# Kernel tuning notes

Measured on AMD Instinct MI355X. Metric: run time of the kernel, lower is better.

Reference implementation:

```python
import jax, jax.numpy as jnp
import numpy as np

B, TQ, TKV, D, H = 4, 1024, 1024, 1024, 16
HD = D // H  # head_size = 64
EPS = 1e-5


def setup_inputs() -> dict:
    key = jax.random.key(0)
    ks = jax.random.split(key, 5)
    s = 0.02
    return {
        "x_q": jax.random.normal(ks[0], (B, TQ, D), jnp.float32),
        "x_kv": jax.random.normal(ks[1], (B, TKV, D), jnp.float32),
        "Wq": jax.random.normal(ks[2], (D, 2 * D), jnp.float32) * s,
        "Wkv": jax.random.normal(ks[3], (D, 3 * D), jnp.float32) * s,
        "Wc": jax.random.normal(ks[4], (D, D), jnp.float32) * s,
        "qn1": jnp.ones((HD,), jnp.float32),
        "kn1": jnp.ones((HD,), jnp.float32),
        "qn2": jnp.ones((HD,), jnp.float32),
        "kn2": jnp.ones((HD,), jnp.float32),
        "gn_w": jnp.ones((D,), jnp.float32),
        "gn_b": jnp.zeros((D,), jnp.float32),
        "lmb": jnp.full((1, H, 1, 1), -4.0, jnp.float32),
    }


def _rms(x, w):
    # RMSNorm over last dim (head_size), eps=1e-5, learned scale w
    return x * jax.lax.rsqrt(jnp.mean(x * x, axis=-1, keepdims=True) + EPS) * w


def _heads(t, T):
    # (B,T,D) -> (B,H,T,HD)
    return t.reshape(B, T, H, HD).transpose(0, 2, 1, 3)


def _attn(q, k, v):
    att = jnp.einsum('bhqd,bhkd->bhqk', q, k) * (1.0 / np.sqrt(HD))
    att = jax.nn.softmax(att, axis=-1)
    return jnp.einsum('bhqk,bhkd->bhqd', att, v)


def reference(x_q, x_kv, Wq, Wkv, Wc, qn1, kn1, qn2, kn2, gn_w, gn_b, lmb):
    q1, q2 = jnp.split(x_q @ Wq, 2, axis=-1)
    k1, k2, v = jnp.split(x_kv @ Wkv, 3, axis=-1)
    q1 = _rms(_heads(q1, TQ), qn1)
    q2 = _rms(_heads(q2, TQ), qn2)
    k1 = _rms(_heads(k1, TKV), kn1)
    k2 = _rms(_heads(k2, TKV), kn2)
    v = _heads(v, TKV)
    y = _attn(q1, k1, v) - jax.nn.softplus(lmb) * _attn(q2, k2, v)  # (B,H,TQ,HD)
    # GroupNorm(n_head groups over n_embd channels), input (B,C,TQ):
    # per (batch, head) stats over (TQ, HD)
    mu = jnp.mean(y, axis=(2, 3), keepdims=True)
    var = jnp.var(y, axis=(2, 3), keepdims=True)
    yn = (y - mu) * jax.lax.rsqrt(var + EPS)
    yn = yn * gn_w.reshape(1, H, 1, HD) + gn_b.reshape(1, H, 1, HD)
    y = yn.transpose(0, 2, 1, 3).reshape(B, TQ, D)
    return y @ Wc
```

## Files before the change

### kernel.cpp

```cpp
#include <hip/hip_runtime.h>
#include <cstdint>
#include <cstddef>

#define B_ 4
#define TQ_ 1024
#define TKV_ 1024
#define D_ 1024
#define H_ 16
#define HD_ 64

typedef __bf16 bf16_t;
typedef bf16_t bf16x4 __attribute__((ext_vector_type(4)));
typedef bf16_t bf16x8 __attribute__((ext_vector_type(8)));
typedef float f32x4 __attribute__((ext_vector_type(4)));

#if __has_builtin(__builtin_amdgcn_exp2f)
#define EXP2F __builtin_amdgcn_exp2f
#else
#define EXP2F exp2f
#endif

__device__ __forceinline__ bf16_t to_bf16(float f) {
  uint32_t u = __builtin_bit_cast(uint32_t, f);
  u += 0x7fffu + ((u >> 16) & 1u);
  uint16_t h = (uint16_t)(u >> 16);
  return __builtin_bit_cast(bf16_t, h);
}
__device__ __forceinline__ float bf2f(bf16_t b) {
  uint32_t u = ((uint32_t)__builtin_bit_cast(uint16_t, b)) << 16;
  return __builtin_bit_cast(float, u);
}
__device__ __forceinline__ uint32_t pack_bf16_trunc(float lo, float hi) {
  return __builtin_amdgcn_perm(__builtin_bit_cast(uint32_t, hi),
                               __builtin_bit_cast(uint32_t, lo), 0x07060302u);
}
__device__ __forceinline__ void gload_lds16(const void* g, void* l) {
  __builtin_amdgcn_global_load_lds((const __attribute__((address_space(1))) void*)g,
                                   (__attribute__((address_space(3))) void*)l, 16, 0, 0);
}

__global__ __launch_bounds__(256) void k_prep(const float* __restrict__ xq,
                                              const float* __restrict__ xkv,
                                              const float* __restrict__ Wq,
                                              const float* __restrict__ Wkv,
                                              const float* __restrict__ Wc,
                                              bf16_t* __restrict__ oq,
                                              bf16_t* __restrict__ okv,
                                              bf16_t* __restrict__ Wqt,
                                              bf16_t* __restrict__ Wkvt,
                                              bf16_t* __restrict__ Wct,
                                              float* __restrict__ part) {
  int blk = blockIdx.x;
  if (blk == 0 && threadIdx.x < 128) part[threadIdx.x] = 0.f;
  if (blk < 8192) {
    const float* in = (blk < 4096) ? xq : xkv;
    bf16_t* out = (blk < 4096) ? oq : okv;
    int i = (blk & 4095) * 256 + threadIdx.x;
    float4 v = ((const float4*)in)[i];
    bf16x4 o = {to_bf16(v.x), to_bf16(v.y), to_bf16(v.z), to_bf16(v.w)};
    *(bf16x4*)(out + (size_t)i * 4) = o;
  } else {
    __shared__ float tile[32][33];
    int t = blk - 8192;
    int x = t % 192, yb = t / 192;
    const float* in;
    bf16_t* out;
    int C, c0;
    if (x < 64) { in = Wq; out = Wqt; C = 2048; c0 = x * 32; }
    else if (x < 160) { in = Wkv; out = Wkvt; C = 3072; c0 = (x - 64) * 32; }
    else { in = Wc; out = Wct; C = 1024; c0 = (x - 160) * 32; }
    int r0 = yb * 32;
    int tx = threadIdx.x & 31, ty = threadIdx.x >> 5;
#pragma unroll
    for (int i = 0; i < 4; i++)
      tile[ty + i * 8][tx] = in[(size_t)(r0 + ty + i * 8) * C + c0 + tx];
    __syncthreads();
#pragma unroll
    for (int i = 0; i < 4; i++) {
      int rr = ty + i * 8;
      out[(size_t)(c0 + rr) * 1024 + r0 + tx] = to_bf16(tile[tx][rr]);
    }
  }
}

__global__ __launch_bounds__(256, 2) void k_gemm_qkv(const bf16_t* __restrict__ xq,
                                                     const bf16_t* __restrict__ xkv,
                                                     const bf16_t* __restrict__ Wqt,
                                                     const bf16_t* __restrict__ Wkvt,
                                                     const float* __restrict__ kn1,
                                                     const float* __restrict__ kn2,
                                                     bf16_t* __restrict__ q12,
                                                     bf16_t* __restrict__ k1h,
                                                     bf16_t* __restrict__ k2h,
                                                     bf16_t* __restrict__ vt) {
  __shared__ bf16_t As[128 * 32];
  __shared__ bf16_t Bs[128 * 32];
  const int tid = threadIdx.x;
  const int wave = tid >> 6, lane = tid & 63;
  const int ln = lane & 15, lq = lane >> 4;

  const int fid = blockIdx.x;
  const int xcd = fid & 7, l = fid >> 3;
  bool isq;
  int xb, yb;
  if (l < 64) {
    isq = true;
    xb = (xcd & 3) * 4 + (l & 3);
    yb = (xcd >> 2) * 16 + (l >> 2);
  } else {
    isq = false;
    int l2 = l - 64;
    xb = (xcd & 3) * 6 + l2 % 6;
    yb = (xcd >> 2) * 16 + l2 / 6;
  }
  const bf16_t* A = isq ? xq : xkv;
  const bf16_t* Bt = isq ? Wqt : Wkvt;
  const int n0 = xb * 128, m0 = yb * 128;
  const int wm = (wave >> 1) * 64, wn = (wave & 1) * 64;
  f32x4 acc[4][4];
#pragma unroll
  for (int i = 0; i < 4; i++)
#pragma unroll
    for (int j = 0; j < 4; j++) acc[i][j] = (f32x4){0.f, 0.f, 0.f, 0.f};

  for (int k0 = 0; k0 < 1024; k0 += 32) {
#pragma unroll
    for (int rnd = 0; rnd < 2; rnd++) {
      int c = rnd * 256 + tid;
      int row = c >> 2, col = (c & 3) * 8;
      int ldsoff = (rnd * 256 + wave * 64) * 16;
      gload_lds16(A + (size_t)(m0 + row) * 1024 + k0 + col, (char*)As + ldsoff);
      gload_lds16(Bt + (size_t)(n0 + row) * 1024 + k0 + col, (char*)Bs + ldsoff);
    }
    asm volatile("s_waitcnt vmcnt(0)" ::: "memory");
    __syncthreads();
    bf16x8 af[4], bfr[4];
#pragma unroll
    for (int i = 0; i < 4; i++) {
      af[i] = *(const bf16x8*)(As + (wm + i * 16 + ln) * 32 + lq * 8);
      bfr[i] = *(const bf16x8*)(Bs + (wn + i * 16 + ln) * 32 + lq * 8);
    }
#pragma unroll
    for (int i = 0; i < 4; i++)
#pragma unroll
      for (int j = 0; j < 4; j++)
        acc[i][j] = __builtin_amdgcn_mfma_f32_16x16x32_bf16(af[i], bfr[j], acc[i][j], 0, 0, 0);
    __syncthreads();
  }

  if (isq) {
#pragma unroll
    for (int i = 0; i < 4; i++)
#pragma unroll
      for (int j = 0; j < 4; j++)
#pragma unroll
        for (int r = 0; r < 4; r++) {
          int row = m0 + wm + i * 16 + lq * 4 + r;
          int col = n0 + wn + j * 16 + ln;
          q12[(size_t)row * 2048 + col] = to_bf16(acc[i][j][r]);
        }
  } else {
    const int col0 = n0 + wn;
    const int part3 = col0 >> 10;
    const int h = (col0 >> 6) & 15;
    const int b = m0 >> 10;
    const int bh = b * 16 + h;
    if (part3 < 2) {
      const float* kn = part3 ? kn2 : kn1;
      bf16_t* dst = part3 ? k2h : k1h;
      float kw[4];
#pragma unroll
      for (int j = 0; j < 4; j++) kw[j] = kn[j * 16 + ln];
#pragma unroll
      for (int i = 0; i < 4; i++)
#pragma unroll
        for (int r = 0; r < 4; r++) {
          float ss = 0.f;
#pragma unroll
          for (int j = 0; j < 4; j++) ss += acc[i][j][r] * acc[i][j][r];
          ss += __shfl_xor(ss, 1, 64);
          ss += __shfl_xor(ss, 2, 64);
          ss += __shfl_xor(ss, 4, 64);
          ss += __shfl_xor(ss, 8, 64);
          float rstd = rsqrtf(ss * (1.f / 64.f) + 1e-5f);
          int m = m0 + wm + i * 16 + lq * 4 + r;
          int t = m & 1023;
          size_t base = ((size_t)bh * 1024 + t) * 64;
#pragma unroll
          for (int j = 0; j < 4; j++)
            dst[base + j * 16 + ln] = to_bf16(acc[i][j][r] * rstd * kw[j]);
        }
    } else {
      bf16_t* obase = vt + (size_t)bh * 65536;
#pragma unroll
      for (int i = 0; i < 4; i++) {
        int t0 = (m0 & 1023) + wm + i * 16 + lq * 4;
#pragma unroll
        for (int j = 0; j < 4; j++) {
          bf16x4 pv;
#pragma unroll
          for (int r = 0; r < 4; r++) pv[r] = to_bf16(acc[i][j][r]);
          *(bf16x4*)(obase + (size_t)(j * 16 + ln) * 1024 + t0) = pv;
        }
      }
    }
  }
}

__global__ __launch_bounds__(256, 2) void k_gemm64(const bf16_t* __restrict__ A,
                                                   const bf16_t* __restrict__ Bt,
                                                   float* __restrict__ C, int N, int K) {
  __shared__ bf16_t As[128 * 32];
  __shared__ bf16_t Bs[64 * 32];
  const int tid = threadIdx.x;
  const int wave = tid >> 6, lane = tid & 63;
  const int ln = lane & 15, lq = lane >> 4;
  const int fid = blockIdx.x;
  const int xcd = fid & 7, l = fid >> 3;
  const int lx = l & 1, ly = (l >> 1) & 15, yh = l >> 5;
  const int n0 = (xcd * 2 + lx) * 64;
  const int m0 = (yh * 16 + ly) * 128;
  const int wm = wave * 32;
  f32x4 acc[2][4];
#pragma unroll
  for (int i = 0; i < 2; i++)
#pragma unroll
    for (int j = 0; j < 4; j++) acc[i][j] = (f32x4){0.f, 0.f, 0.f, 0.f};

  for (int k0 = 0; k0 < K; k0 += 32) {
#pragma unroll
    for (int rnd = 0; rnd < 2; rnd++) {
      int c = rnd * 256 + tid;
      int row = c >> 2, col = (c & 3) * 8;
      int ldsoff = (rnd * 256 + wave * 64) * 16;
      gload_lds16(A + (size_t)(m0 + row) * K + k0 + col, (char*)As + ldsoff);
    }
    {
      int row = tid >> 2, col = (tid & 3) * 8;
      int ldsoff = (wave * 64) * 16;
      gload_lds16(Bt + (size_t)(n0 + row) * K + k0 + col, (char*)Bs + ldsoff);
    }
    asm volatile("s_waitcnt vmcnt(0)" ::: "memory");
    __syncthreads();
    bf16x8 af[2], bfr[4];
#pragma unroll
    for (int i = 0; i < 2; i++)
      af[i] = *(const bf16x8*)(As + (wm + i * 16 + ln) * 32 + lq * 8);
#pragma unroll
    for (int j = 0; j < 4; j++)
      bfr[j] = *(const bf16x8*)(Bs + (j * 16 + ln) * 32 + lq * 8);
#pragma unroll
    for (int i = 0; i < 2; i++)
#pragma unroll
      for (int j = 0; j < 4; j++)
        acc[i][j] = __builtin_amdgcn_mfma_f32_16x16x32_bf16(af[i], bfr[j], acc[i][j], 0, 0, 0);
    __syncthreads();
  }
#pragma unroll
  for (int i = 0; i < 2; i++)
#pragma unroll
    for (int j = 0; j < 4; j++)
#pragma unroll
      for (int r = 0; r < 4; r++) {
        int row = m0 + wm + i * 16 + lq * 4 + r;
        int col = n0 + j * 16 + ln;
        C[(size_t)row * N + col] = acc[i][j][r];
      }
}

__global__ __launch_bounds__(256, 4) void k_attn2(const bf16_t* __restrict__ q12,
                                                  const bf16_t* __restrict__ k1h,
                                                  const bf16_t* __restrict__ k2h,
                                                  const bf16_t* __restrict__ vt,
                                                  const float* __restrict__ qn1,
                                                  const float* __restrict__ qn2,
                                                  const float* __restrict__ lmb,
                                                  bf16_t* __restrict__ y,
                                                  float* __restrict__ part) {
  __shared__ bf16_t Ks[2][4096];
  __shared__ bf16_t Vs[4096];
  const int tid = threadIdx.x;
  const int wave = tid >> 6, lane = tid & 63;
  const int ln = lane & 15, lq = lane >> 4;
  const int swz = ln & 7;
  const int bh = blockIdx.x;
  const int b = bh >> 4, h = bh & 15;
  const int q0 = blockIdx.y * 64 + wave * 16;
  const bf16_t* kb[2] = {k1h + (size_t)bh * 65536, k2h + (size_t)bh * 65536};
  const bf16_t* vb = vt + (size_t)bh * 65536;

  bf16x8 qf[2][2];
#pragma unroll
  for (int st = 0; st < 2; st++)
#pragma unroll
    for (int ks = 0; ks < 2; ks++)
      qf[st][ks] = *(const bf16x8*)(q12 + (size_t)(b * 1024 + q0 + ln) * 2048 + st * 1024 +
                                    h * 64 + ks * 32 + lq * 8);
#pragma unroll
  for (int st = 0; st < 2; st++) {
    const float* qn = st ? qn2 : qn1;
    float ssq = 0.f;
#pragma unroll
    for (int ks = 0; ks < 2; ks++)
#pragma unroll
      for (int j = 0; j < 8; j++) {
        float v = bf2f(qf[st][ks][j]);
        ssq += v * v;
      }
    ssq += __shfl_xor(ssq, 16, 64);
    ssq += __shfl_xor(ssq, 32, 64);
    float rr = rsqrtf(ssq * (1.f / 64.f) + 1e-5f) * (0.125f * 1.44269504f);
#pragma unroll
    for (int ks = 0; ks < 2; ks++)
#pragma unroll
      for (int j = 0; j < 8; j++)
        qf[st][ks][j] = to_bf16(bf2f(qf[st][ks][j]) * rr * qn[ks * 32 + lq * 8 + j]);
  }

  f32x4 O[2][4];
  float lp[2] = {0.f, 0.f};
#pragma unroll
  for (int st = 0; st < 2; st++)
#pragma unroll
    for (int nt = 0; nt < 4; nt++) O[st][nt] = (f32x4){0.f, 0.f, 0.f, 0.f};

  for (int kv0 = 0; kv0 < TKV_; kv0 += 64) {
    __syncthreads();
#pragma unroll
    for (int r = 0; r < 6; r++) {
      int a = r >> 1, r2 = r & 1;
      int g = r2 * 256 + tid;
      int row = g >> 3;
      int blk = (g & 7) ^ (row & 7);
      const bf16_t* src = (a < 2) ? (kb[a] + (size_t)(kv0 + row) * 64 + blk * 8)
                                  : (vb + (size_t)row * 1024 + kv0 + blk * 8);
      char* dst = (a < 2) ? ((char*)Ks + a * 8192) : (char*)Vs;
      gload_lds16(src, dst + (r2 * 256 + wave * 64) * 16);
    }
    asm volatile("s_waitcnt vmcnt(0)" ::: "memory");
    __syncthreads();

#pragma unroll
    for (int st = 0; st < 2; st++) {
      bf16x8 kf[2][4];
#pragma unroll
      for (int ks = 0; ks < 2; ks++)
#pragma unroll
        for (int t = 0; t < 4; t++)
          kf[ks][t] = *(const bf16x8*)(&Ks[st][((t * 16 + ln) * 8 + ((4 * ks + lq) ^ swz)) * 8]);
      f32x4 s[4];
#pragma unroll
      for (int t = 0; t < 4; t++) s[t] = (f32x4){0.f, 0.f, 0.f, 0.f};
#pragma unroll
      for (int ks = 0; ks < 2; ks++)
#pragma unroll
        for (int t = 0; t < 4; t++)
          s[t] = __builtin_amdgcn_mfma_f32_16x16x32_bf16(kf[ks][t], qf[st][ks], s[t], 0, 0, 0);
      uint32_t pfu[2][4];
      float l = 0.f;
#pragma unroll
      for (int t = 0; t < 4; t++) {
        float e0 = EXP2F(s[t][0]), e1 = EXP2F(s[t][1]);
        float e2 = EXP2F(s[t][2]), e3 = EXP2F(s[t][3]);
        l += (e0 + e1) + (e2 + e3);
        pfu[t >> 1][(t & 1) * 2] = pack_bf16_trunc(e0, e1);
        pfu[t >> 1][(t & 1) * 2 + 1] = pack_bf16_trunc(e2, e3);
      }
      lp[st] += l;
#pragma unroll
      for (int u = 0; u < 2; u++) {
        bf16x8 pf = __builtin_bit_cast(bf16x8, *(uint4*)pfu[u]);
#pragma unroll
        for (int nt = 0; nt < 4; nt++) {
          uint2 lo = *(const uint2*)(Vs + ((nt * 16 + ln) * 8 + ((u * 4 + (lq >> 1)) ^ swz)) * 8 +
                                     (lq & 1) * 4);
          uint2 hi = *(const uint2*)(Vs + ((nt * 16 + ln) * 8 + ((u * 4 + 2 + (lq >> 1)) ^ swz)) * 8 +
                                     (lq & 1) * 4);
          uint4 vq = {lo.x, lo.y, hi.x, hi.y};
          bf16x8 vfrag = __builtin_bit_cast(bf16x8, vq);
          O[st][nt] = __builtin_amdgcn_mfma_f32_16x16x32_bf16(pf, vfrag, O[st][nt], 0, 0, 0);
        }
      }
    }
  }

  float c = log1pf(__expf(lmb[h]));
  float linv[2][4];
#pragma unroll
  for (int st = 0; st < 2; st++) {
    float l = lp[st];
    l += __shfl_xor(l, 16, 64);
    l += __shfl_xor(l, 32, 64);
#pragma unroll
    for (int r = 0; r < 4; r++) linv[st][r] = 1.f / __shfl(l, lq * 4 + r, 64);
  }
  float s_acc = 0.f, ss_acc = 0.f;
#pragma unroll
  for (int nt = 0; nt < 4; nt++)
#pragma unroll
    for (int r = 0; r < 4; r++) {
      size_t a = ((size_t)bh * TQ_ + q0 + lq * 4 + r) * 64 + nt * 16 + ln;
      float val = O[0][nt][r] * linv[0][r] - c * O[1][nt][r] * linv[1][r];
      s_acc += val;
      ss_acc += val * val;
      y[a] = to_bf16(val);
    }
#pragma unroll
  for (int m = 1; m < 64; m <<= 1) {
    s_acc += __shfl_xor(s_acc, m, 64);
    ss_acc += __shfl_xor(ss_acc, m, 64);
  }
  if (lane == 0) {
    atomicAdd(&part[bh * 2], s_acc);
    atomicAdd(&part[bh * 2 + 1], ss_acc);
  }
}

__global__ __launch_bounds__(256) void k_gn_apply(const bf16_t* __restrict__ y,
                                                  const float* __restrict__ part,
                                                  const float* __restrict__ gw,
                                                  const float* __restrict__ gb,
                                                  bf16_t* __restrict__ yn) {
  int idx = blockIdx.x * 256 + threadIdx.x;
  int i = idx * 8;
  int bh = i >> 16;
  int h = bh & 15, b = bh >> 4;
  float S = part[bh * 2], SS = part[bh * 2 + 1];
  float mean = S * (1.f / 65536.f);
  float var = SS * (1.f / 65536.f) - mean * mean;
  float rstd = rsqrtf(var + 1e-5f);
  bf16x8 a = *(const bf16x8*)(y + i);
  int rem = i & 65535;
  int t = rem >> 6, d = rem & 63;
  bf16x8 o;
#pragma unroll
  for (int j = 0; j < 8; j++) {
    float f = (bf2f(a[j]) - mean) * rstd * gw[h * 64 + d + j] + gb[h * 64 + d + j];
    o[j] = to_bf16(f);
  }
  *(bf16x8*)(yn + ((size_t)(b * 1024 + t)) * 1024 + h * 64 + d) = o;
}

extern "C" void kernel_launch(void* const* d_in, const int* in_sizes, int n_in,
                              void* d_out, int out_size, void* d_ws, size_t ws_size,
                              hipStream_t stream) {
  const float* x_q = (const float*)d_in[0];
  const float* x_kv = (const float*)d_in[1];
  const float* Wq = (const float*)d_in[2];
  const float* Wkv = (const float*)d_in[3];
  const float* Wc = (const float*)d_in[4];
  const float* qn1 = (const float*)d_in[5];
  const float* kn1 = (const float*)d_in[6];
  const float* qn2 = (const float*)d_in[7];
  const float* kn2 = (const float*)d_in[8];
  const float* gn_w = (const float*)d_in[9];
  const float* gn_b = (const float*)d_in[10];
  const float* lmb = (const float*)d_in[11];

  const size_t MB = (size_t)1 << 20;
  char* ws = (char*)d_ws;
  bf16_t* xq_bf = (bf16_t*)(ws + 0 * MB);
  bf16_t* xkv_bf = (bf16_t*)(ws + 8 * MB);
  bf16_t* Wqt = (bf16_t*)(ws + 16 * MB);
  bf16_t* Wkvt = (bf16_t*)(ws + 20 * MB);
  bf16_t* Wct = (bf16_t*)(ws + 26 * MB);
  bf16_t* q12 = (bf16_t*)(ws + 28 * MB);
  bf16_t* k1h = (bf16_t*)(ws + 44 * MB);
  bf16_t* k2h = (bf16_t*)(ws + 52 * MB);
  bf16_t* vt = (bf16_t*)(ws + 60 * MB);
  bf16_t* y = (bf16_t*)(ws + 68 * MB);
  bf16_t* yn = (bf16_t*)(ws + 76 * MB);
  float* part = (float*)(ws + 84 * MB);

  k_prep<<<14336, 256, 0, stream>>>(x_q, x_kv, Wq, Wkv, Wc, xq_bf, xkv_bf, Wqt, Wkvt, Wct,
                                    part);
  k_gemm_qkv<<<1280, 256, 0, stream>>>(xq_bf, xkv_bf, Wqt, Wkvt, kn1, kn2, q12, k1h, k2h,
                                       vt);
  k_attn2<<<dim3(64, 16), 256, 0, stream>>>(q12, k1h, k2h, vt, qn1, qn2, lmb, y, part);
  k_gn_apply<<<2048, 256, 0, stream>>>(y, part, gn_w, gn_b, yn);
  k_gemm64<<<512, 256, 0, stream>>>(yn, Wct, (float*)d_out, 1024, 1024);
}
```

Before: 268.6 us.

## Double per-wave query rows in attention and pre-permute V for single LDS reads

Each attention wave now handles 32 query rows instead of 16, so every K and V tile staged in shared memory is reused across two query sub-tiles, and the grid is halved to match. The V-transpose writer in the QKV GEMM stores columns in a permuted order so the attention kernel can fetch each V fragment with one 16-byte LDS read instead of two 8-byte reads, with V fragments hoisted out of the score loop. GroupNorm partial sums are first reduced across waves in shared memory, leaving one atomic per block. The trade-off is more registers per thread (occupancy hint lowered from 4 to 2) and fewer blocks available to fill the GPU.

Result: faster. 238.3 us (-11.3%).

```diff
diff --git a/kernel.cpp b/kernel.cpp
--- a/kernel.cpp
+++ b/kernel.cpp
@@ -195,12 +195,13 @@
 #pragma unroll
       for (int i = 0; i < 4; i++) {
         int t0 = (m0 & 1023) + wm + i * 16 + lq * 4;
+        int tp = (t0 & ~31) | (((t0 >> 2) & 3) << 3) | (((t0 >> 4) & 1) << 2);
 #pragma unroll
         for (int j = 0; j < 4; j++) {
           bf16x4 pv;
 #pragma unroll
           for (int r = 0; r < 4; r++) pv[r] = to_bf16(acc[i][j][r]);
-          *(bf16x4*)(obase + (size_t)(j * 16 + ln) * 1024 + t0) = pv;
+          *(bf16x4*)(obase + (size_t)(j * 16 + ln) * 1024 + tp) = pv;
         }
       }
     }
@@ -268,7 +269,7 @@
       }
 }
 
-__global__ __launch_bounds__(256, 4) void k_attn2(const bf16_t* __restrict__ q12,
+__global__ __launch_bounds__(256, 2) void k_attn2(const bf16_t* __restrict__ q12,
                                                   const bf16_t* __restrict__ k1h,
                                                   const bf16_t* __restrict__ k2h,
                                                   const bf16_t* __restrict__ vt,
@@ -279,50 +280,57 @@
                                                   float* __restrict__ part) {
   __shared__ bf16_t Ks[2][4096];
   __shared__ bf16_t Vs[4096];
+  __shared__ float red[8];
   const int tid = threadIdx.x;
   const int wave = tid >> 6, lane = tid & 63;
   const int ln = lane & 15, lq = lane >> 4;
   const int swz = ln & 7;
   const int bh = blockIdx.x;
   const int b = bh >> 4, h = bh & 15;
-  const int q0 = blockIdx.y * 64 + wave * 16;
+  const int q0 = blockIdx.y * 128 + wave * 32;
   const bf16_t* kb[2] = {k1h + (size_t)bh * 65536, k2h + (size_t)bh * 65536};
   const bf16_t* vb = vt + (size_t)bh * 65536;
 
-  bf16x8 qf[2][2];
+  bf16x8 qf[2][2][2];
 #pragma unroll
   for (int st = 0; st < 2; st++)
 #pragma unroll
-    for (int ks = 0; ks < 2; ks++)
-      qf[st][ks] = *(const bf16x8*)(q12 + (size_t)(b * 1024 + q0 + ln) * 2048 + st * 1024 +
-                                    h * 64 + ks * 32 + lq * 8);
-#pragma unroll
-  for (int st = 0; st < 2; st++) {
-    const float* qn = st ? qn2 : qn1;
-    float ssq = 0.f;
-#pragma unroll
-    for (int ks = 0; ks < 2; ks++)
-#pragma unroll
-      for (int j = 0; j < 8; j++) {
-        float v = bf2f(qf[st][ks][j]);
-        ssq += v * v;
-      }
-    ssq += __shfl_xor(ssq, 16, 64);
-    ssq += __shfl_xor(ssq, 32, 64);
-    float rr = rsqrtf(ssq * (1.f / 64.f) + 1e-5f) * (0.125f * 1.44269504f);
-#pragma unroll
-    for (int ks = 0; ks < 2; ks++)
-#pragma unroll
-      for (int j = 0; j < 8; j++)
-        qf[st][ks][j] = to_bf16(bf2f(qf[st][ks][j]) * rr * qn[ks * 32 + lq * 8 + j]);
-  }
-
-  f32x4 O[2][4];
-  float lp[2] = {0.f, 0.f};
+    for (int mt = 0; mt < 2; mt++)
+#pragma unroll
+      for (int ks = 0; ks < 2; ks++)
+        qf[st][mt][ks] = *(const bf16x8*)(q12 + (size_t)(b * 1024 + q0 + mt * 16 + ln) * 2048 +
+                                          st * 1024 + h * 64 + ks * 32 + lq * 8);
 #pragma unroll
   for (int st = 0; st < 2; st++)
 #pragma unroll
-    for (int nt = 0; nt < 4; nt++) O[st][nt] = (f32x4){0.f, 0.f, 0.f, 0.f};
+    for (int mt = 0; mt < 2; mt++) {
+      const float* qn = st ? qn2 : qn1;
+      float ssq = 0.f;
+#pragma unroll
+      for (int ks = 0; ks < 2; ks++)
+#pragma unroll
+        for (int j = 0; j < 8; j++) {
+          float v = bf2f(qf[st][mt][ks][j]);
+          ssq += v * v;
+        }
+      ssq += __shfl_xor(ssq, 16, 64);
+      ssq += __shfl_xor(ssq, 32, 64);
+      float rr = rsqrtf(ssq * (1.f / 64.f) + 1e-5f) * (0.125f * 1.44269504f);
+#pragma unroll
+      for (int ks = 0; ks < 2; ks++)
+#pragma unroll
+        for (int j = 0; j < 8; j++)
+          qf[st][mt][ks][j] = to_bf16(bf2f(qf[st][mt][ks][j]) * rr * qn[ks * 32 + lq * 8 + j]);
+    }
+
+  f32x4 O[2][2][4];
+  float lp[2][2] = {{0.f, 0.f}, {0.f, 0.f}};
+#pragma unroll
+  for (int st = 0; st < 2; st++)
+#pragma unroll
+    for (int mt = 0; mt < 2; mt++)
+#pragma unroll
+      for (int nt = 0; nt < 4; nt++) O[st][mt][nt] = (f32x4){0.f, 0.f, 0.f, 0.f};
 
   for (int kv0 = 0; kv0 < TKV_; kv0 += 64) {
     __syncthreads();
@@ -340,6 +348,13 @@
     asm volatile("s_waitcnt vmcnt(0)" ::: "memory");
     __syncthreads();
 
+    bf16x8 vf[2][4];
+#pragma unroll
+    for (int u = 0; u < 2; u++)
+#pragma unroll
+      for (int nt = 0; nt < 4; nt++)
+        vf[u][nt] = *(const bf16x8*)(Vs + ((nt * 16 + ln) * 8 + ((u * 4 + lq) ^ swz)) * 8);
+
 #pragma unroll
     for (int st = 0; st < 2; st++) {
       bf16x8 kf[2][4];
@@ -348,71 +363,76 @@
 #pragma unroll
         for (int t = 0; t < 4; t++)
           kf[ks][t] = *(const bf16x8*)(&Ks[st][((t * 16 + ln) * 8 + ((4 * ks + lq) ^ swz)) * 8]);
-      f32x4 s[4];
-#pragma unroll
-      for (int t = 0; t < 4; t++) s[t] = (f32x4){0.f, 0.f, 0.f, 0.f};
-#pragma unroll
-      for (int ks = 0; ks < 2; ks++)
-#pragma unroll
-        for (int t = 0; t < 4; t++)
-          s[t] = __builtin_amdgcn_mfma_f32_16x16x32_bf16(kf[ks][t], qf[st][ks], s[t], 0, 0, 0);
-      uint32_t pfu[2][4];
-      float l = 0.f;
-#pragma unroll
-      for (int t = 0; t < 4; t++) {
-        float e0 = EXP2F(s[t][0]), e1 = EXP2F(s[t][1]);
-        float e2 = EXP2F(s[t][2]), e3 = EXP2F(s[t][3]);
-        l += (e0 + e1) + (e2 + e3);
-        pfu[t >> 1][(t & 1) * 2] = pack_bf16_trunc(e0, e1);
-        pfu[t >> 1][(t & 1) * 2 + 1] = pack_bf16_trunc(e2, e3);
-      }
-      lp[st] += l;
-#pragma unroll
-      for (int u = 0; u < 2; u++) {
-        bf16x8 pf = __builtin_bit_cast(bf16x8, *(uint4*)pfu[u]);
-#pragma unroll
-        for (int nt = 0; nt < 4; nt++) {
-          uint2 lo = *(const uint2*)(Vs + ((nt * 16 + ln) * 8 + ((u * 4 + (lq >> 1)) ^ swz)) * 8 +
-                                     (lq & 1) * 4);
-          uint2 hi = *(const uint2*)(Vs + ((nt * 16 + ln) * 8 + ((u * 4 + 2 + (lq >> 1)) ^ swz)) * 8 +
-                                     (lq & 1) * 4);
-          uint4 vq = {lo.x, lo.y, hi.x, hi.y};
-          bf16x8 vfrag = __builtin_bit_cast(bf16x8, vq);
-          O[st][nt] = __builtin_amdgcn_mfma_f32_16x16x32_bf16(pf, vfrag, O[st][nt], 0, 0, 0);
+#pragma unroll
+      for (int mt = 0; mt < 2; mt++) {
+        f32x4 s[4];
+#pragma unroll
+        for (int t = 0; t < 4; t++) s[t] = (f32x4){0.f, 0.f, 0.f, 0.f};
+#pragma unroll
+        for (int ks = 0; ks < 2; ks++)
+#pragma unroll
+          for (int t = 0; t < 4; t++)
+            s[t] = __builtin_amdgcn_mfma_f32_16x16x32_bf16(kf[ks][t], qf[st][mt][ks], s[t], 0, 0, 0);
+        uint32_t pfu[2][4];
+        float l = 0.f;
+#pragma unroll
+        for (int t = 0; t < 4; t++) {
+          float e0 = EXP2F(s[t][0]), e1 = EXP2F(s[t][1]);
+          float e2 = EXP2F(s[t][2]), e3 = EXP2F(s[t][3]);
+          l += (e0 + e1) + (e2 + e3);
+          pfu[t >> 1][(t & 1) * 2] = pack_bf16_trunc(e0, e1);
+          pfu[t >> 1][(t & 1) * 2 + 1] = pack_bf16_trunc(e2, e3);
+        }
+        lp[st][mt] += l;
+#pragma unroll
+        for (int u = 0; u < 2; u++) {
+          bf16x8 pf = __builtin_bit_cast(bf16x8, *(uint4*)pfu[u]);
+#pragma unroll
+          for (int nt = 0; nt < 4; nt++)
+            O[st][mt][nt] =
+                __builtin_amdgcn_mfma_f32_16x16x32_bf16(pf, vf[u][nt], O[st][mt][nt], 0, 0, 0);
         }
       }
     }
   }
 
   float c = log1pf(__expf(lmb[h]));
-  float linv[2][4];
-#pragma unroll
-  for (int st = 0; st < 2; st++) {
-    float l = lp[st];
-    l += __shfl_xor(l, 16, 64);
-    l += __shfl_xor(l, 32, 64);
-#pragma unroll
-    for (int r = 0; r < 4; r++) linv[st][r] = 1.f / __shfl(l, lq * 4 + r, 64);
-  }
   float s_acc = 0.f, ss_acc = 0.f;
 #pragma unroll
-  for (int nt = 0; nt < 4; nt++)
-#pragma unroll
-    for (int r = 0; r < 4; r++) {
-      size_t a = ((size_t)bh * TQ_ + q0 + lq * 4 + r) * 64 + nt * 16 + ln;
-      float val = O[0][nt][r] * linv[0][r] - c * O[1][nt][r] * linv[1][r];
-      s_acc += val;
-      ss_acc += val * val;
-      y[a] = to_bf16(val);
-    }
+  for (int mt = 0; mt < 2; mt++) {
+    float linv[2][4];
+#pragma unroll
+    for (int st = 0; st < 2; st++) {
+      float l = lp[st][mt];
+      l += __shfl_xor(l, 16, 64);
+      l += __shfl_xor(l, 32, 64);
+#pragma unroll
+      for (int r = 0; r < 4; r++) linv[st][r] = 1.f / __shfl(l, lq * 4 + r, 64);
+    }
+#pragma unroll
+    for (int nt = 0; nt < 4; nt++)
+#pragma unroll
+      for (int r = 0; r < 4; r++) {
+        size_t a = ((size_t)bh * TQ_ + q0 + mt * 16 + lq * 4 + r) * 64 + nt * 16 + ln;
+        float val = O[0][mt][nt][r] * linv[0][r] - c * O[1][mt][nt][r] * linv[1][r];
+        s_acc += val;
+        ss_acc += val * val;
+        y[a] = to_bf16(val);
+      }
+  }
 #pragma unroll
   for (int m = 1; m < 64; m <<= 1) {
     s_acc += __shfl_xor(s_acc, m, 64);
     ss_acc += __shfl_xor(ss_acc, m, 64);
   }
   if (lane == 0) {
-    atomicAdd(&part[bh * 2], s_acc);
-    atomicAdd(&part[bh * 2 + 1], ss_acc);
+    red[wave] = s_acc;
+    red[4 + wave] = ss_acc;
+  }
+  __syncthreads();
+  if (tid == 0) {
+    atomicAdd(&part[bh * 2], red[0] + red[1] + red[2] + red[3]);
+    atomicAdd(&part[bh * 2 + 1], red[4] + red[5] + red[6] + red[7]);
   }
 }
 
@@ -476,7 +496,7 @@
                                     part);
   k_gemm_qkv<<<1280, 256, 0, stream>>>(xq_bf, xkv_bf, Wqt, Wkvt, kn1, kn2, q12, k1h, k2h,
                                        vt);
-  k_attn2<<<dim3(64, 16), 256, 0, stream>>>(q12, k1h, k2h, vt, qn1, qn2, lmb, y, part);
+  k_attn2<<<dim3(64, 8), 256, 0, stream>>>(q12, k1h, k2h, vt, qn1, qn2, lmb, y, part);
   k_gn_apply<<<2048, 256, 0, stream>>>(y, part, gn_w, gn_b, yn);
   k_gemm64<<<512, 256, 0, stream>>>(yn, Wct, (float*)d_out, 1024, 1024);
 }
```
